# Performance work log

Hardware: AMD Instinct MI355X
Metric: run time of the kernel (lower is better)

The kernel has to match this reference:

```python
import jax, jax.numpy as jnp
import numpy as np

N_NODES = 100000
N_EDGES = 2400000


def setup_inputs() -> dict:
    key = jax.random.key(0)
    ks = jax.random.split(key, 8)
    x = jax.random.normal(ks[0], (N_NODES, 1), dtype=jnp.float32)
    edge_index = jax.random.randint(ks[1], (2, N_EDGES), 0, N_NODES, dtype=jnp.int64)
    # GCNConv weights: lin (in, out) and bias (out,), glorot-ish init
    def w(k, fan_in, fan_out):
        return jax.random.normal(k, (fan_in, fan_out), dtype=jnp.float32) / np.sqrt(fan_in)
    return {
        "x": x,
        "edge_index": edge_index,
        "W1": w(ks[2], 1, 32), "b1": jnp.zeros((32,), jnp.float32),
        "W2": w(ks[3], 32, 16), "b2": jnp.zeros((16,), jnp.float32),
        "W3": w(ks[4], 16, 1), "b3": jnp.zeros((1,), jnp.float32),
    }


def _gcn_conv(x, W, b, src, dst, norm, n):
    # x: [N, Fin] -> linear first (cheaper), then gather-scale-scatter
    h = x @ W                                   # [N, Fout]
    msg = h[src] * norm[:, None]                # [E+N, Fout] gather on src
    out = jax.ops.segment_sum(msg, dst, num_segments=n)  # scatter-add on dst
    return out + b


def reference(x, edge_index, W1, b1, W2, b2, W3, b3):
    n = x.shape[0]
    loops = jnp.arange(n, dtype=edge_index.dtype)
    src = jnp.concatenate([edge_index[0], loops])  # PyG: add self-loops
    dst = jnp.concatenate([edge_index[1], loops])
    # symmetric normalization: deg computed on targets with unit edge weights
    deg = jax.ops.segment_sum(jnp.ones_like(src, dtype=x.dtype), dst, num_segments=n)
    dis = jnp.where(deg > 0, jax.lax.rsqrt(deg), 0.0)
    norm = dis[src] * dis[dst]                  # [E+N]
    h = jax.nn.relu(_gcn_conv(x, W1, b1, src, dst, norm, n))
    h = jax.nn.relu(_gcn_conv(h, W2, b2, src, dst, norm, n))
    return _gcn_conv(h, W3, b3, src, dst, norm, n)
```

## Files before the change

### kernel.cpp

```cpp
#include <hip/hip_runtime.h>
#include <hip/hip_fp16.h>

static constexpr int NN   = 100000;
static constexpr int NE   = 2400000;
static constexpr int MSH  = 9;
static constexpr unsigned MMSK = 511;
static constexpr int NND  = 512;
static constexpr int MBN  = (NN + 511) / 512;
static constexpr int CAPM = 13184;
static constexpr int NPB  = 1024;
static constexpr int SEG  = 2344;
static_assert((size_t)NPB * SEG >= NE, "segments cover edge list");
static_assert(SEG % 4 == 0 && NE % 4 == 0 && CAPM % 4 == 0, "uint4 alignment");
static_assert(MBN <= 256, "mid hist fits one pass");
static_assert(NN % 32 == 0, "8-lane-per-node kernels assume NN % 32 == 0");

__global__ __launch_bounds__(256) void khistM(const int* __restrict__ dst,
                                              unsigned* __restrict__ H) {
    __shared__ unsigned h[MBN];
    int b = blockIdx.x, t = threadIdx.x;
    for (int k = t; k < MBN; k += 256) h[k] = 0;
    __syncthreads();
    int off = b * SEG;
    int n = NE - off; if (n > SEG) n = SEG; if (n < 0) n = 0;
    for (int j = 4 * t; j + 3 < n; j += 1024) {
        uint4 d4 = *reinterpret_cast<const uint4*>(dst + off + j);
        atomicAdd(&h[d4.x >> MSH], 1u);
        atomicAdd(&h[d4.y >> MSH], 1u);
        atomicAdd(&h[d4.z >> MSH], 1u);
        atomicAdd(&h[d4.w >> MSH], 1u);
    }
    __syncthreads();
    for (int k = t; k < MBN; k += 256) H[(size_t)b * MBN + k] = h[k];
}

__global__ __launch_bounds__(1024) void kscanM(const unsigned* __restrict__ H,
                                               unsigned* __restrict__ P,
                                               unsigned* __restrict__ cntM) {
    __shared__ unsigned a[1024], b2[1024];
    int k = blockIdx.x, t = threadIdx.x;
    unsigned v = H[(size_t)t * MBN + k];
    a[t] = v;
    __syncthreads();
    unsigned* cu = a; unsigned* nx = b2;
    for (int o = 1; o < 1024; o <<= 1) {
        unsigned x = cu[t];
        if (t >= o) x += cu[t - o];
        nx[t] = x;
        __syncthreads();
        unsigned* tm = cu; cu = nx; nx = tm;
    }
    P[(size_t)k * NPB + t] = cu[t] - v;
    if (t == 1023) cntM[k] = cu[t];
}

__global__ __launch_bounds__(256) void kscatterM(const int* __restrict__ src,
                                                 const int* __restrict__ dst,
                                                 const unsigned* __restrict__ P,
                                                 unsigned* __restrict__ csr) {
    __shared__ unsigned lcur[MBN];
    int b = blockIdx.x, t = threadIdx.x;
    for (int k = t; k < MBN; k += 256)
        lcur[k] = (unsigned)k * CAPM + P[(size_t)k * NPB + b];
    __syncthreads();
    int off = b * SEG;
    int n = NE - off; if (n > SEG) n = SEG; if (n < 0) n = 0;
    for (int j = 4 * t; j + 3 < n; j += 1024) {
        uint4 d4 = *reinterpret_cast<const uint4*>(dst + off + j);
        uint4 s4 = *reinterpret_cast<const uint4*>(src + off + j);
        unsigned p0 = atomicAdd(&lcur[d4.x >> MSH], 1u);
        csr[p0] = (s4.x << MSH) | (d4.x & MMSK);
        unsigned p1 = atomicAdd(&lcur[d4.y >> MSH], 1u);
        csr[p1] = (s4.y << MSH) | (d4.y & MMSK);
        unsigned p2 = atomicAdd(&lcur[d4.z >> MSH], 1u);
        csr[p2] = (s4.z << MSH) | (d4.z & MMSK);
        unsigned p3 = atomicAdd(&lcur[d4.w >> MSH], 1u);
        csr[p3] = (s4.w << MSH) | (d4.w & MMSK);
    }
}

__global__ __launch_bounds__(512) void kcsrB2(const unsigned* __restrict__ csr,
                                              const unsigned* __restrict__ cntM,
                                              const float* __restrict__ x,
                                              unsigned* __restrict__ csr2,
                                              unsigned* __restrict__ rstart,
                                              unsigned* __restrict__ rcnt,
                                              float* __restrict__ dis,
                                              float* __restrict__ y1) {
    __shared__ __align__(16) unsigned codes[CAPM];
    __shared__ int cnt[NND];
    __shared__ unsigned ps1[NND], ps2[NND];
    __shared__ unsigned cur[NND];
    int m = blockIdx.x, t = threadIdx.x;
    unsigned sbase = (unsigned)m * CAPM;
    unsigned nM = cntM[m]; if (nM > CAPM) nM = CAPM;
    cnt[t] = 0;
    __syncthreads();
    unsigned nM4 = nM & ~3u;
    for (unsigned j = 4u * t; j < nM4; j += 2048) {
        uint4 c4 = *reinterpret_cast<const uint4*>(csr + sbase + j);
        *reinterpret_cast<uint4*>(&codes[j]) = c4;
        atomicAdd(&cnt[c4.x & MMSK], 1);
        atomicAdd(&cnt[c4.y & MMSK], 1);
        atomicAdd(&cnt[c4.z & MMSK], 1);
        atomicAdd(&cnt[c4.w & MMSK], 1);
    }
    for (unsigned j = nM4 + t; j < nM; j += 512) {
        unsigned c = csr[sbase + j];
        codes[j] = c;
        atomicAdd(&cnt[c & MMSK], 1);
    }
    __syncthreads();
    unsigned v = (unsigned)cnt[t];
    ps1[t] = v;
    __syncthreads();
    unsigned* cu = ps1; unsigned* nx = ps2;
    for (int o = 1; o < 512; o <<= 1) {
        unsigned s = cu[t];
        if (t >= o) s += cu[t - o];
        nx[t] = s;
        __syncthreads();
        unsigned* tm = cu; cu = nx; nx = tm;
    }
    unsigned excl = cu[t] - v;
    cur[t] = excl;
    int node = m * NND + t;
    if (node < NN) {
        rstart[node] = sbase + excl;
        rcnt[node] = v;
        float d = rsqrtf((float)((int)v + 1));
        dis[node] = d;
        y1[node] = d * x[node];
    }
    __syncthreads();
    for (unsigned j = t; j < nM; j += 512) {
        unsigned c = codes[j];
        unsigned pos = atomicAdd(&cur[c & MMSK], 1u);
        csr2[sbase + pos] = c >> MSH;
    }
}


__global__ __launch_bounds__(256) void kagg1lin(const unsigned* __restrict__ srcs,
                                                const unsigned* __restrict__ rstart,
                                                const unsigned* __restrict__ rcnt,
                                                const float* __restrict__ y1,
                                                const float* __restrict__ dis,
                                                const float* __restrict__ W1,
                                                const float* __restrict__ b1,
                                                const float* __restrict__ W2,
                                                __half* __restrict__ y2) {
    __shared__ float sW1[32], sb1[32], sW2[512];
    int t = threadIdx.x;
    if (t < 32) { sW1[t] = W1[t]; sb1[t] = b1[t]; }
    for (int i = t; i < 512; i += 256) sW2[i] = W2[i];
    __syncthreads();
    int node = blockIdx.x * 16 + (t >> 4);
    int g = t & 15;
    unsigned r0 = rstart[node], r1 = r0 + rcnt[node];
    float s0 = 0.f, s1 = 0.f;
    unsigned j = r0 + g;
    for (; j + 16 < r1; j += 32) {
        unsigned i0 = srcs[j], i1 = srcs[j + 16];
        float v0 = y1[i0], v1 = y1[i1];
        s0 += v0; s1 += v1;
    }
    if (j < r1) s0 += y1[srcs[j]];
    float sum = s0 + s1;
    sum += __shfl_xor(sum, 1, 16);
    sum += __shfl_xor(sum, 2, 16);
    sum += __shfl_xor(sum, 4, 16);
    sum += __shfl_xor(sum, 8, 16);
    float d = dis[node];
    float a = d * (sum + y1[node]);
    float acc = 0.f;
#pragma unroll
    for (int f = 0; f < 32; ++f) {
        float h = fmaxf(a * sW1[f] + sb1[f], 0.f);
        acc += h * sW2[f * 16 + g];
    }
    y2[(size_t)node * 16 + g] = __float2half(d * acc);
}

__global__ __launch_bounds__(256) void kagg16g(const unsigned* __restrict__ srcs,
                                               const unsigned* __restrict__ rstart,
                                               const unsigned* __restrict__ rcnt,
                                               const __half2* __restrict__ y2,
                                               const float* __restrict__ dis,
                                               const float* __restrict__ b2,
                                               const float* __restrict__ W3,
                                               float* __restrict__ y3) {
    int t = threadIdx.x;
    int node = blockIdx.x * 32 + (t >> 3);
    int l = t & 7;
    unsigned r0 = rstart[node], r1 = r0 + rcnt[node];
    const __half2* yl = y2 + l;
    float sx0 = 0.f, sy0 = 0.f, sx1 = 0.f, sy1 = 0.f;
    float sx2 = 0.f, sy2 = 0.f, sx3 = 0.f, sy3 = 0.f;
    unsigned j = r0;
    for (; j + 8 <= r1; j += 8) {
        unsigned i0 = srcs[j + 0], i1 = srcs[j + 1], i2 = srcs[j + 2], i3 = srcs[j + 3];
        unsigned i4 = srcs[j + 4], i5 = srcs[j + 5], i6 = srcs[j + 6], i7 = srcs[j + 7];
        float2 v0 = __half22float2(yl[(size_t)i0 * 8]);
        float2 v1 = __half22float2(yl[(size_t)i1 * 8]);
        float2 v2 = __half22float2(yl[(size_t)i2 * 8]);
        float2 v3 = __half22float2(yl[(size_t)i3 * 8]);
        float2 v4 = __half22float2(yl[(size_t)i4 * 8]);
        float2 v5 = __half22float2(yl[(size_t)i5 * 8]);
        float2 v6 = __half22float2(yl[(size_t)i6 * 8]);
        float2 v7 = __half22float2(yl[(size_t)i7 * 8]);
        sx0 += v0.x; sy0 += v0.y; sx1 += v1.x; sy1 += v1.y;
        sx2 += v2.x; sy2 += v2.y; sx3 += v3.x; sy3 += v3.y;
        sx0 += v4.x; sy0 += v4.y; sx1 += v5.x; sy1 += v5.y;
        sx2 += v6.x; sy2 += v6.y; sx3 += v7.x; sy3 += v7.y;
    }
    for (; j + 2 <= r1; j += 2) {
        unsigned i0 = srcs[j], i1 = srcs[j + 1];
        float2 v0 = __half22float2(yl[(size_t)i0 * 8]);
        float2 v1 = __half22float2(yl[(size_t)i1 * 8]);
        sx0 += v0.x; sy0 += v0.y; sx1 += v1.x; sy1 += v1.y;
    }
    if (j < r1) {
        float2 v = __half22float2(yl[(size_t)srcs[j] * 8]);
        sx2 += v.x; sy2 += v.y;
    }
    float sumx = (sx0 + sx1) + (sx2 + sx3);
    float sumy = (sy0 + sy1) + (sy2 + sy3);
    float d = dis[node];
    float2 self = __half22float2(yl[(size_t)node * 8]);
    float ax = d * (sumx + self.x) + b2[2 * l];
    float ay = d * (sumy + self.y) + b2[2 * l + 1];
    float hg = fmaxf(ax, 0.f) * W3[2 * l] + fmaxf(ay, 0.f) * W3[2 * l + 1];
    hg += __shfl_xor(hg, 1, 8);
    hg += __shfl_xor(hg, 2, 8);
    hg += __shfl_xor(hg, 4, 8);
    if (l == 0) y3[node] = d * hg;
}

__global__ __launch_bounds__(256) void kaggsg(const unsigned* __restrict__ srcs,
                                              const unsigned* __restrict__ rstart,
                                              const unsigned* __restrict__ rcnt,
                                              const float* __restrict__ y,
                                              const float* __restrict__ dis,
                                              float* __restrict__ out,
                                              const float* __restrict__ bias) {
    int t = threadIdx.x;
    int node = blockIdx.x * 32 + (t >> 3);
    int l = t & 7;
    unsigned r0 = rstart[node], r1 = r0 + rcnt[node];
    float s0 = 0.f, s1 = 0.f;
    unsigned j = r0 + l;
    for (; j + 8 < r1; j += 16) {
        unsigned i0 = srcs[j], i1 = srcs[j + 8];
        float v0 = y[i0], v1 = y[i1];
        s0 += v0; s1 += v1;
    }
    if (j < r1) s0 += y[srcs[j]];
    float sum = s0 + s1;
    sum += __shfl_xor(sum, 1, 8);
    sum += __shfl_xor(sum, 2, 8);
    sum += __shfl_xor(sum, 4, 8);
    if (l == 0) {
        float d = dis[node];
        out[node] = d * (sum + y[node]) + (bias ? bias[0] : 0.f);
    }
}

extern "C" void kernel_launch(void* const* d_in, const int* in_sizes, int n_in,
                              void* d_out, int out_size, void* d_ws, size_t ws_size,
                              hipStream_t stream) {
    const float* x  = (const float*)d_in[0];
    const int*   ei = (const int*)d_in[1];
    const int* src = ei;
    const int* dst = ei + NE;
    const float* W1 = (const float*)d_in[2];
    const float* b1 = (const float*)d_in[3];
    const float* W2 = (const float*)d_in[4];
    const float* b2 = (const float*)d_in[5];
    const float* W3 = (const float*)d_in[6];
    const float* b3 = (const float*)d_in[7];
    float* out = (float*)d_out;

    auto align256 = [](size_t v) { return (v + 255) & ~(size_t)255; };
    char* w = (char*)d_ws;
    auto carve = [&](size_t bytes) { char* p = w; w += align256(bytes); return p; };

    char* regA = carve((size_t)MBN * CAPM * 4);
    unsigned* csr = (unsigned*)regA;
    __half*   y2  = (__half*)regA;
    unsigned* csr2   = (unsigned*)carve((size_t)MBN * CAPM * 4);
    unsigned* H      = (unsigned*)carve((size_t)NPB * MBN * 4);
    unsigned* P      = (unsigned*)carve((size_t)MBN * NPB * 4);
    unsigned* cntM   = (unsigned*)carve((size_t)MBN * 4);
    unsigned* rstart = (unsigned*)carve((size_t)NN * 4);
    unsigned* rcnt   = (unsigned*)carve((size_t)NN * 4);
    float*    dis    = (float*)   carve((size_t)NN * 4);
    float*    y1     = (float*)   carve((size_t)NN * 4);
    float*    y3     = (float*)   carve((size_t)NN * 4);

    dim3 B(256);

    khistM   <<<NPB, B, 0, stream>>>(dst, H);
    kscanM   <<<MBN, dim3(1024), 0, stream>>>(H, P, cntM);
    kscatterM<<<NPB, B, 0, stream>>>(src, dst, P, csr);
    kcsrB2   <<<MBN, dim3(512), 0, stream>>>(csr, cntM, x, csr2, rstart, rcnt, dis, y1);

    kagg1lin<<<NN / 16, B, 0, stream>>>(csr2, rstart, rcnt, y1, dis, W1, b1, W2, y2);

    kagg16g <<<NN / 32, B, 0, stream>>>(csr2, rstart, rcnt, (const __half2*)y2,
                                        dis, b2, W3, y3);

    kaggsg  <<<NN / 32, B, 0, stream>>>(csr2, rstart, rcnt, y3, dis, out, b3);
}
```

Before: 97.60 us.

## Replace hist/scan/scatter partition with single-pass atomic cursor bucketing

The three-kernel coarse partition (per-block histogram, 1024-wide scan, scatter) becomes one kernel. Each block histograms its edge segment, reserves space in every bucket with one global atomicAdd on a per-bucket cursor, then scatters into that space. This drops two launches and the H/P round trips. Edge order inside a bucket now depends on atomic timing, which may affect float summation order. Separately, kagg1lin now uses 8 lanes per node and writes half2 pairs, with 32 nodes per block.

```diff
diff --git a/kernel.cpp b/kernel.cpp
--- a/kernel.cpp
+++ b/kernel.cpp
@@ -15,72 +15,53 @@
 static_assert(MBN <= 256, "mid hist fits one pass");
 static_assert(NN % 32 == 0, "8-lane-per-node kernels assume NN % 32 == 0");
 
-__global__ __launch_bounds__(256) void khistM(const int* __restrict__ dst,
-                                              unsigned* __restrict__ H) {
-    __shared__ unsigned h[MBN];
+__global__ __launch_bounds__(256) void kinit(unsigned* __restrict__ cursor) {
+    int i = threadIdx.x;
+    if (i < MBN) cursor[i] = (unsigned)i * CAPM;
+}
+
+__global__ __launch_bounds__(256) void kpartA(const int* __restrict__ src,
+                                              const int* __restrict__ dst,
+                                              unsigned* __restrict__ cursor,
+                                              unsigned* __restrict__ csr) {
+    __shared__ unsigned hist[MBN];
+    __shared__ unsigned gb[MBN];
     int b = blockIdx.x, t = threadIdx.x;
-    for (int k = t; k < MBN; k += 256) h[k] = 0;
+    for (int k = t; k < MBN; k += 256) hist[k] = 0;
     __syncthreads();
     int off = b * SEG;
     int n = NE - off; if (n > SEG) n = SEG; if (n < 0) n = 0;
     for (int j = 4 * t; j + 3 < n; j += 1024) {
         uint4 d4 = *reinterpret_cast<const uint4*>(dst + off + j);
-        atomicAdd(&h[d4.x >> MSH], 1u);
-        atomicAdd(&h[d4.y >> MSH], 1u);
-        atomicAdd(&h[d4.z >> MSH], 1u);
-        atomicAdd(&h[d4.w >> MSH], 1u);
-    }
-    __syncthreads();
-    for (int k = t; k < MBN; k += 256) H[(size_t)b * MBN + k] = h[k];
-}
-
-__global__ __launch_bounds__(1024) void kscanM(const unsigned* __restrict__ H,
-                                               unsigned* __restrict__ P,
-                                               unsigned* __restrict__ cntM) {
-    __shared__ unsigned a[1024], b2[1024];
-    int k = blockIdx.x, t = threadIdx.x;
-    unsigned v = H[(size_t)t * MBN + k];
-    a[t] = v;
-    __syncthreads();
-    unsigned* cu = a; unsigned* nx = b2;
-    for (int o = 1; o < 1024; o <<= 1) {
-        unsigned x = cu[t];
-        if (t >= o) x += cu[t - o];
-        nx[t] = x;
-        __syncthreads();
-        unsigned* tm = cu; cu = nx; nx = tm;
-    }
-    P[(size_t)k * NPB + t] = cu[t] - v;
-    if (t == 1023) cntM[k] = cu[t];
-}
-
-__global__ __launch_bounds__(256) void kscatterM(const int* __restrict__ src,
-                                                 const int* __restrict__ dst,
-                                                 const unsigned* __restrict__ P,
-                                                 unsigned* __restrict__ csr) {
-    __shared__ unsigned lcur[MBN];
-    int b = blockIdx.x, t = threadIdx.x;
-    for (int k = t; k < MBN; k += 256)
-        lcur[k] = (unsigned)k * CAPM + P[(size_t)k * NPB + b];
-    __syncthreads();
-    int off = b * SEG;
-    int n = NE - off; if (n > SEG) n = SEG; if (n < 0) n = 0;
+        atomicAdd(&hist[d4.x >> MSH], 1u);
+        atomicAdd(&hist[d4.y >> MSH], 1u);
+        atomicAdd(&hist[d4.z >> MSH], 1u);
+        atomicAdd(&hist[d4.w >> MSH], 1u);
+    }
+    __syncthreads();
+    if (t < MBN) {
+        unsigned c = hist[t];
+        gb[t] = c ? atomicAdd(&cursor[t], c) : 0u;
+    }
+    __syncthreads();
+    if (t < MBN) hist[t] = 0;
+    __syncthreads();
     for (int j = 4 * t; j + 3 < n; j += 1024) {
         uint4 d4 = *reinterpret_cast<const uint4*>(dst + off + j);
         uint4 s4 = *reinterpret_cast<const uint4*>(src + off + j);
-        unsigned p0 = atomicAdd(&lcur[d4.x >> MSH], 1u);
-        csr[p0] = (s4.x << MSH) | (d4.x & MMSK);
-        unsigned p1 = atomicAdd(&lcur[d4.y >> MSH], 1u);
-        csr[p1] = (s4.y << MSH) | (d4.y & MMSK);
-        unsigned p2 = atomicAdd(&lcur[d4.z >> MSH], 1u);
-        csr[p2] = (s4.z << MSH) | (d4.z & MMSK);
-        unsigned p3 = atomicAdd(&lcur[d4.w >> MSH], 1u);
-        csr[p3] = (s4.w << MSH) | (d4.w & MMSK);
+        unsigned k0 = d4.x >> MSH;
+        csr[gb[k0] + atomicAdd(&hist[k0], 1u)] = (s4.x << MSH) | (d4.x & MMSK);
+        unsigned k1 = d4.y >> MSH;
+        csr[gb[k1] + atomicAdd(&hist[k1], 1u)] = (s4.y << MSH) | (d4.y & MMSK);
+        unsigned k2 = d4.z >> MSH;
+        csr[gb[k2] + atomicAdd(&hist[k2], 1u)] = (s4.z << MSH) | (d4.z & MMSK);
+        unsigned k3 = d4.w >> MSH;
+        csr[gb[k3] + atomicAdd(&hist[k3], 1u)] = (s4.w << MSH) | (d4.w & MMSK);
     }
 }
 
 __global__ __launch_bounds__(512) void kcsrB2(const unsigned* __restrict__ csr,
-                                              const unsigned* __restrict__ cntM,
+                                              const unsigned* __restrict__ cursor,
                                               const float* __restrict__ x,
                                               unsigned* __restrict__ csr2,
                                               unsigned* __restrict__ rstart,
@@ -93,7 +74,7 @@
     __shared__ unsigned cur[NND];
     int m = blockIdx.x, t = threadIdx.x;
     unsigned sbase = (unsigned)m * CAPM;
-    unsigned nM = cntM[m]; if (nM > CAPM) nM = CAPM;
+    unsigned nM = cursor[m] - sbase; if (nM > CAPM) nM = CAPM;
     cnt[t] = 0;
     __syncthreads();
     unsigned nM4 = nM & ~3u;
@@ -149,37 +130,37 @@
                                                 const float* __restrict__ W1,
                                                 const float* __restrict__ b1,
                                                 const float* __restrict__ W2,
-                                                __half* __restrict__ y2) {
+                                                __half2* __restrict__ y2) {
     __shared__ float sW1[32], sb1[32], sW2[512];
     int t = threadIdx.x;
     if (t < 32) { sW1[t] = W1[t]; sb1[t] = b1[t]; }
     for (int i = t; i < 512; i += 256) sW2[i] = W2[i];
     __syncthreads();
-    int node = blockIdx.x * 16 + (t >> 4);
-    int g = t & 15;
+    int node = blockIdx.x * 32 + (t >> 3);
+    int l = t & 7;
     unsigned r0 = rstart[node], r1 = r0 + rcnt[node];
     float s0 = 0.f, s1 = 0.f;
-    unsigned j = r0 + g;
-    for (; j + 16 < r1; j += 32) {
-        unsigned i0 = srcs[j], i1 = srcs[j + 16];
+    unsigned j = r0 + l;
+    for (; j + 8 < r1; j += 16) {
+        unsigned i0 = srcs[j], i1 = srcs[j + 8];
         float v0 = y1[i0], v1 = y1[i1];
         s0 += v0; s1 += v1;
     }
     if (j < r1) s0 += y1[srcs[j]];
     float sum = s0 + s1;
-    sum += __shfl_xor(sum, 1, 16);
-    sum += __shfl_xor(sum, 2, 16);
-    sum += __shfl_xor(sum, 4, 16);
-    sum += __shfl_xor(sum, 8, 16);
+    sum += __shfl_xor(sum, 1, 8);
+    sum += __shfl_xor(sum, 2, 8);
+    sum += __shfl_xor(sum, 4, 8);
     float d = dis[node];
     float a = d * (sum + y1[node]);
-    float acc = 0.f;
+    float acc0 = 0.f, acc1 = 0.f;
 #pragma unroll
     for (int f = 0; f < 32; ++f) {
         float h = fmaxf(a * sW1[f] + sb1[f], 0.f);
-        acc += h * sW2[f * 16 + g];
-    }
-    y2[(size_t)node * 16 + g] = __float2half(d * acc);
+        acc0 += h * sW2[f * 16 + 2 * l];
+        acc1 += h * sW2[f * 16 + 2 * l + 1];
+    }
+    y2[(size_t)node * 8 + l] = __floats2half2_rn(d * acc0, d * acc1);
 }
 
 __global__ __launch_bounds__(256) void kagg16g(const unsigned* __restrict__ srcs,
@@ -287,11 +268,9 @@
 
     char* regA = carve((size_t)MBN * CAPM * 4);
     unsigned* csr = (unsigned*)regA;
-    __half*   y2  = (__half*)regA;
+    __half2*  y2  = (__half2*)regA;
     unsigned* csr2   = (unsigned*)carve((size_t)MBN * CAPM * 4);
-    unsigned* H      = (unsigned*)carve((size_t)NPB * MBN * 4);
-    unsigned* P      = (unsigned*)carve((size_t)MBN * NPB * 4);
-    unsigned* cntM   = (unsigned*)carve((size_t)MBN * 4);
+    unsigned* cursor = (unsigned*)carve((size_t)MBN * 4);
     unsigned* rstart = (unsigned*)carve((size_t)NN * 4);
     unsigned* rcnt   = (unsigned*)carve((size_t)NN * 4);
     float*    dis    = (float*)   carve((size_t)NN * 4);
@@ -300,15 +279,13 @@
 
     dim3 B(256);
 
-    khistM   <<<NPB, B, 0, stream>>>(dst, H);
-    kscanM   <<<MBN, dim3(1024), 0, stream>>>(H, P, cntM);
-    kscatterM<<<NPB, B, 0, stream>>>(src, dst, P, csr);
-    kcsrB2   <<<MBN, dim3(512), 0, stream>>>(csr, cntM, x, csr2, rstart, rcnt, dis, y1);
-
-    kagg1lin<<<NN / 16, B, 0, stream>>>(csr2, rstart, rcnt, y1, dis, W1, b1, W2, y2);
-
-    kagg16g <<<NN / 32, B, 0, stream>>>(csr2, rstart, rcnt, (const __half2*)y2,
-                                        dis, b2, W3, y3);
+    kinit <<<1, B, 0, stream>>>(cursor);
+    kpartA<<<NPB, B, 0, stream>>>(src, dst, cursor, csr);
+    kcsrB2<<<MBN, dim3(512), 0, stream>>>(csr, cursor, x, csr2, rstart, rcnt, dis, y1);
+
+    kagg1lin<<<NN / 32, B, 0, stream>>>(csr2, rstart, rcnt, y1, dis, W1, b1, W2, y2);
+
+    kagg16g <<<NN / 32, B, 0, stream>>>(csr2, rstart, rcnt, y2, dis, b2, W3, y3);
 
     kaggsg  <<<NN / 32, B, 0, stream>>>(csr2, rstart, rcnt, y3, dis, out, b3);
 }
```

Measured after the change: 110.8 us. 13.5% more time.
